# Optimization experiments

Measured on AMD Instinct MI355X. Metric: run time of the kernel, lower is better.

The kernel has to match this reference:

```python
import jax, jax.numpy as jnp
import numpy as np

B, CH_IN, CH_LAT, CLASSES, H, W = 4, 128, 128, 128, 1, 131072
BN_EPS = 1e-5
NEG_SLOPE = 0.01  # torch F.leaky_relu default


def setup_inputs() -> dict:
    key = jax.random.key(0)
    ks = jax.random.split(key, 12)
    x = jax.random.normal(ks[0], (B, CH_IN, H, W), jnp.float32)
    # 1x1 convs stored as [out_ch, in_ch]
    conv1_w = jax.random.normal(ks[1], (CH_LAT, CH_IN), jnp.float32) / np.sqrt(CH_IN).astype(np.float32)
    conv1_b = jax.random.normal(ks[2], (CH_LAT,), jnp.float32) * 0.1
    bn_gamma = jax.random.uniform(ks[3], (CH_LAT,), jnp.float32, 0.5, 1.5)
    bn_beta = jax.random.normal(ks[4], (CH_LAT,), jnp.float32) * 0.1
    bn_mean = jax.random.normal(ks[5], (CH_LAT,), jnp.float32) * 0.1
    bn_var = jax.random.uniform(ks[6], (CH_LAT,), jnp.float32, 0.5, 1.5)
    conv2_w = jax.random.normal(ks[7], (CLASSES + 1, CH_LAT), jnp.float32) / np.sqrt(CH_LAT).astype(np.float32)
    conv2_b = jax.random.normal(ks[8], (CLASSES + 1,), jnp.float32) * 0.1
    # CondMul: per-class weight [classes, in_feat] (output_features=1) + bias [classes]
    cm_w = jax.random.normal(ks[9], (CLASSES, CH_LAT), jnp.float32) / np.sqrt(CH_LAT).astype(np.float32)
    cm_b = jax.random.normal(ks[10], (CLASSES,), jnp.float32) * 0.1
    return {"x": x, "conv1_w": conv1_w, "conv1_b": conv1_b,
            "bn_gamma": bn_gamma, "bn_beta": bn_beta, "bn_mean": bn_mean, "bn_var": bn_var,
            "conv2_w": conv2_w, "conv2_b": conv2_b, "cm_w": cm_w, "cm_b": cm_b}


def reference(x, conv1_w, conv1_b, bn_gamma, bn_beta, bn_mean, bn_var,
              conv2_w, conv2_b, cm_w, cm_b):
    C = cm_w.shape[0]
    # conv_1 (1x1) + BatchNorm (eval, running stats) + LeakyReLU
    h = jnp.einsum('bchw,oc->bohw', x, conv1_w) + conv1_b[None, :, None, None]
    scale = bn_gamma * jax.lax.rsqrt(bn_var + BN_EPS)
    h = (h - bn_mean[None, :, None, None]) * scale[None, :, None, None] + bn_beta[None, :, None, None]
    x_latent = jnp.where(h >= 0, h, NEG_SLOPE * h)  # [B, CH_LAT, H, W]
    # conv_2 (1x1): classes logits + mask channel
    y = jnp.einsum('bchw,oc->bohw', x_latent, conv2_w) + conv2_b[None, :, None, None]
    cls_logits = y[:, :C]                              # [B, classes, H, W]
    m = y[:, -1:]
    mask = jnp.where(m >= 0, m, NEG_SLOPE * m)          # [B, 1, H, W]
    # tokens: transpose(1,3).reshape(-1, C) as in torch (valid since H==1)
    bsz, cl = x_latent.shape[0], x_latent.shape[1]
    x_l = jnp.transpose(x_latent, (0, 3, 2, 1)).reshape(-1, cl)  # [B*W*H, CH_LAT]
    inds = jnp.argmax(cls_logits, axis=1)               # [B, H, W] int
    idx = inds.reshape(-1)
    # CondMul: per-token class-indexed weight gather + dot product (irregular access)
    reg = jnp.sum(x_l * cm_w[idx], axis=1) + cm_b[idx]   # [B*H*W]
    reg = reg.reshape(bsz, 1, 1, -1)                     # [B, 1, 1, H*W]
    out = (inds[:, None].astype(jnp.float32) + reg) * (1.0 / float(C))
    return out, mask
```

## Files before the change

kernel.cpp:

```cpp
#include <hip/hip_runtime.h>
#include <math.h>

constexpr int CH   = 128;
constexpr int WW   = 131072;
constexpr int NB   = 4;
constexpr int NPIX = NB * WW;
constexpr int TPB  = 256;

constexpr int OFF_W1T = 0;
constexpr int OFF_BNA = 16384;
constexpr int OFF_BNC = 16512;
constexpr int OFF_W2G = 16640;
constexpr int OFF_WM  = 33024;

__global__ __launch_bounds__(256) void prep_kernel(
    const float* __restrict__ w1, const float* __restrict__ b1,
    const float* __restrict__ gamma, const float* __restrict__ beta,
    const float* __restrict__ mean, const float* __restrict__ var,
    const float* __restrict__ w2,
    float* __restrict__ ws)
{
    const int tid = threadIdx.x;
    for (int i = tid; i < CH * CH; i += 256) {
        const int c = i >> 7, o = i & 127;
        ws[OFF_W1T + c * CH + o] = w1[o * CH + c];
    }
    if (tid < CH) {
        const float s = gamma[tid] / sqrtf(var[tid] + 1e-5f);
        ws[OFF_BNA + tid] = s;
        ws[OFF_BNC + tid] = (b1[tid] - mean[tid]) * s + beta[tid];
        ws[OFF_WM  + tid] = w2[CH * CH + tid];
    }
    for (int i = tid; i < 16 * CH * 8; i += 256) {
        const int rg = i >> 10, r = i & 1023, c = r >> 3, j = r & 7;
        ws[OFF_W2G + i] = w2[(rg * 8 + j) * CH + c];
    }
}

__global__ __launch_bounds__(TPB, 2) void fused_kernel(
    const float* __restrict__ x,
    const float* __restrict__ b2,
    const float* __restrict__ cmw,
    const float* __restrict__ cmb,
    const float* __restrict__ ws,
    float* __restrict__ out)
{
    const int tid = threadIdx.x;
    const int p   = blockIdx.x * TPB + tid;
    const int b   = p >> 17;
    const int w   = p & (WW - 1);

    const float* __restrict__ w1t = ws + OFF_W1T;
    const float* __restrict__ bnA = ws + OFF_BNA;
    const float* __restrict__ bnC = ws + OFF_BNC;
    const float* __restrict__ w2g = ws + OFF_W2G;
    const float* __restrict__ wm  = ws + OFF_WM;

    float acc[CH];
    #pragma unroll
    for (int o = 0; o < CH; ++o) acc[o] = 0.f;

    const float* xc = x + ((size_t)b * CH) * WW + w;
    #pragma unroll 4
    for (int c = 0; c < CH; ++c) {
        const float xv = xc[(size_t)c * WW];
        const float* __restrict__ wr = w1t + c * CH;
        #pragma unroll
        for (int o = 0; o < CH; ++o)
            acc[o] = fmaf(xv, wr[o], acc[o]);
    }

    #pragma unroll
    for (int o = 0; o < CH; ++o) {
        const float v = fmaf(acc[o], bnA[o], bnC[o]);
        acc[o] = (v >= 0.f) ? v : 0.01f * v;
    }

    float best = -3.0e38f;
    int   bidx = 0;
    #pragma unroll 1
    for (int rg = 0; rg < 16; ++rg) {
        float y[8];
        #pragma unroll
        for (int j = 0; j < 8; ++j) y[j] = b2[rg * 8 + j];
        const float* __restrict__ wg = w2g + rg * (CH * 8);
        #pragma unroll
        for (int c = 0; c < CH; ++c) {
            #pragma unroll
            for (int j = 0; j < 8; ++j)
                y[j] = fmaf(acc[c], wg[c * 8 + j], y[j]);
        }
        #pragma unroll
        for (int j = 0; j < 8; ++j) {
            const bool g = y[j] > best;
            best = g ? y[j] : best;
            bidx = g ? rg * 8 + j : bidx;
        }
    }

    {
        float m = b2[CH];
        #pragma unroll
        for (int c = 0; c < CH; ++c)
            m = fmaf(acc[c], wm[c], m);
        out[NPIX + p] = (m >= 0.f) ? m : 0.01f * m;
    }

    {
        const float4* __restrict__ cr = (const float4*)(cmw + (size_t)bidx * CH);
        float r0 = 0.f, r1 = 0.f, r2 = 0.f, r3 = 0.f;
        #pragma unroll
        for (int c4 = 0; c4 < 32; ++c4) {
            const float4 v = cr[c4];
            r0 = fmaf(acc[c4*4+0], v.x, r0);
            r1 = fmaf(acc[c4*4+1], v.y, r1);
            r2 = fmaf(acc[c4*4+2], v.z, r2);
            r3 = fmaf(acc[c4*4+3], v.w, r3);
        }
        const float reg = ((r0 + r1) + (r2 + r3)) + cmb[bidx];
        out[p] = ((float)bidx + reg) * (1.0f / 128.0f);
    }
}

extern "C" void kernel_launch(void* const* d_in, const int* in_sizes, int n_in,
                              void* d_out, int out_size, void* d_ws, size_t ws_size,
                              hipStream_t stream) {
    const float* x     = (const float*)d_in[0];
    const float* w1    = (const float*)d_in[1];
    const float* b1    = (const float*)d_in[2];
    const float* gamma = (const float*)d_in[3];
    const float* beta  = (const float*)d_in[4];
    const float* mean  = (const float*)d_in[5];
    const float* var   = (const float*)d_in[6];
    const float* w2    = (const float*)d_in[7];
    const float* b2    = (const float*)d_in[8];
    const float* cmw   = (const float*)d_in[9];
    const float* cmb   = (const float*)d_in[10];
    float* ws  = (float*)d_ws;
    float* out = (float*)d_out;

    hipLaunchKernelGGL(prep_kernel, dim3(1), dim3(256), 0, stream,
                       w1, b1, gamma, beta, mean, var, w2, ws);
    hipLaunchKernelGGL(fused_kernel, dim3(NPIX / TPB), dim3(TPB), 0, stream,
                       x, b2, cmw, cmb, ws, out);
}
```

Before: 1.055 ms.

## Stage conv weights in LDS and prefetch input channels in groups of eight

Each block now copies both transposed 1x1-conv weight matrices (128 KB in total) into shared memory and reads them as float4 from LDS instead of through scalar global/constant loads. The input channel loop is restructured to software-prefetch the next eight channels while computing the current eight. Block size goes to 512 with occupancy 1, and the prep kernel is spread over 64 blocks. The 128 KB of LDS per block limits occupancy to one block per CU, and every block pays a fresh weight copy.

```diff
diff --git a/kernel.cpp b/kernel.cpp
--- a/kernel.cpp
+++ b/kernel.cpp
@@ -5,12 +5,12 @@
 constexpr int WW   = 131072;
 constexpr int NB   = 4;
 constexpr int NPIX = NB * WW;
-constexpr int TPB  = 256;
+constexpr int TPB  = 512;
 
 constexpr int OFF_W1T = 0;
-constexpr int OFF_BNA = 16384;
-constexpr int OFF_BNC = 16512;
-constexpr int OFF_W2G = 16640;
+constexpr int OFF_W2G = 16384;
+constexpr int OFF_BNA = 32768;
+constexpr int OFF_BNC = 32896;
 constexpr int OFF_WM  = 33024;
 
 __global__ __launch_bounds__(256) void prep_kernel(
@@ -20,24 +20,25 @@
     const float* __restrict__ w2,
     float* __restrict__ ws)
 {
-    const int tid = threadIdx.x;
-    for (int i = tid; i < CH * CH; i += 256) {
+    const int gid    = blockIdx.x * 256 + threadIdx.x;
+    const int stride = gridDim.x * 256;
+    for (int i = gid; i < CH * CH; i += stride) {
         const int c = i >> 7, o = i & 127;
         ws[OFF_W1T + c * CH + o] = w1[o * CH + c];
     }
-    if (tid < CH) {
-        const float s = gamma[tid] / sqrtf(var[tid] + 1e-5f);
-        ws[OFF_BNA + tid] = s;
-        ws[OFF_BNC + tid] = (b1[tid] - mean[tid]) * s + beta[tid];
-        ws[OFF_WM  + tid] = w2[CH * CH + tid];
-    }
-    for (int i = tid; i < 16 * CH * 8; i += 256) {
+    for (int i = gid; i < 16 * CH * 8; i += stride) {
         const int rg = i >> 10, r = i & 1023, c = r >> 3, j = r & 7;
         ws[OFF_W2G + i] = w2[(rg * 8 + j) * CH + c];
     }
+    if (gid < CH) {
+        const float s = gamma[gid] / sqrtf(var[gid] + 1e-5f);
+        ws[OFF_BNA + gid] = s;
+        ws[OFF_BNC + gid] = (b1[gid] - mean[gid]) * s + beta[gid];
+        ws[OFF_WM  + gid] = w2[CH * CH + gid];
+    }
 }
 
-__global__ __launch_bounds__(TPB, 2) void fused_kernel(
+__global__ __launch_bounds__(TPB, 1) void fused_kernel(
     const float* __restrict__ x,
     const float* __restrict__ b2,
     const float* __restrict__ cmw,
@@ -45,15 +46,29 @@
     const float* __restrict__ ws,
     float* __restrict__ out)
 {
+    __shared__ float lw1[CH * CH];
+    __shared__ float lw2[16 * CH * 8];
+
     const int tid = threadIdx.x;
-    const int p   = blockIdx.x * TPB + tid;
-    const int b   = p >> 17;
-    const int w   = p & (WW - 1);
 
-    const float* __restrict__ w1t = ws + OFF_W1T;
+    {
+        const float4* __restrict__ s1 = (const float4*)(ws + OFF_W1T);
+        float4* d1 = (float4*)lw1;
+        #pragma unroll
+        for (int k = 0; k < 8; ++k) d1[k * TPB + tid] = s1[k * TPB + tid];
+        const float4* __restrict__ s2 = (const float4*)(ws + OFF_W2G);
+        float4* d2 = (float4*)lw2;
+        #pragma unroll
+        for (int k = 0; k < 8; ++k) d2[k * TPB + tid] = s2[k * TPB + tid];
+    }
+    __syncthreads();
+
+    const int p = blockIdx.x * TPB + tid;
+    const int b = p >> 17;
+    const int w = p & (WW - 1);
+
     const float* __restrict__ bnA = ws + OFF_BNA;
     const float* __restrict__ bnC = ws + OFF_BNC;
-    const float* __restrict__ w2g = ws + OFF_W2G;
     const float* __restrict__ wm  = ws + OFF_WM;
 
     float acc[CH];
@@ -61,13 +76,42 @@
     for (int o = 0; o < CH; ++o) acc[o] = 0.f;
 
     const float* xc = x + ((size_t)b * CH) * WW + w;
-    #pragma unroll 4
-    for (int c = 0; c < CH; ++c) {
-        const float xv = xc[(size_t)c * WW];
-        const float* __restrict__ wr = w1t + c * CH;
+    float xa[8], xnx[8];
+    #pragma unroll
+    for (int k = 0; k < 8; ++k) xa[k] = xc[(size_t)k * WW];
+
+    #pragma unroll 1
+    for (int cg = 0; cg < CH - 8; cg += 8) {
         #pragma unroll
-        for (int o = 0; o < CH; ++o)
-            acc[o] = fmaf(xv, wr[o], acc[o]);
+        for (int k = 0; k < 8; ++k) xnx[k] = xc[(size_t)(cg + 8 + k) * WW];
+        #pragma unroll
+        for (int k = 0; k < 8; ++k) {
+            const float xv = xa[k];
+            const float4* __restrict__ wr = (const float4*)&lw1[(cg + k) * CH];
+            #pragma unroll
+            for (int o4 = 0; o4 < 32; ++o4) {
+                const float4 w4 = wr[o4];
+                acc[o4*4+0] = fmaf(xv, w4.x, acc[o4*4+0]);
+                acc[o4*4+1] = fmaf(xv, w4.y, acc[o4*4+1]);
+                acc[o4*4+2] = fmaf(xv, w4.z, acc[o4*4+2]);
+                acc[o4*4+3] = fmaf(xv, w4.w, acc[o4*4+3]);
+            }
+        }
+        #pragma unroll
+        for (int k = 0; k < 8; ++k) xa[k] = xnx[k];
+    }
+    #pragma unroll
+    for (int k = 0; k < 8; ++k) {
+        const float xv = xa[k];
+        const float4* __restrict__ wr = (const float4*)&lw1[(120 + k) * CH];
+        #pragma unroll
+        for (int o4 = 0; o4 < 32; ++o4) {
+            const float4 w4 = wr[o4];
+            acc[o4*4+0] = fmaf(xv, w4.x, acc[o4*4+0]);
+            acc[o4*4+1] = fmaf(xv, w4.y, acc[o4*4+1]);
+            acc[o4*4+2] = fmaf(xv, w4.z, acc[o4*4+2]);
+            acc[o4*4+3] = fmaf(xv, w4.w, acc[o4*4+3]);
+        }
     }
 
     #pragma unroll
@@ -83,12 +127,19 @@
         float y[8];
         #pragma unroll
         for (int j = 0; j < 8; ++j) y[j] = b2[rg * 8 + j];
-        const float* __restrict__ wg = w2g + rg * (CH * 8);
+        const float* __restrict__ wg = &lw2[rg * (CH * 8)];
         #pragma unroll
         for (int c = 0; c < CH; ++c) {
-            #pragma unroll
-            for (int j = 0; j < 8; ++j)
-                y[j] = fmaf(acc[c], wg[c * 8 + j], y[j]);
+            const float4 wa = *(const float4*)&wg[c * 8];
+            const float4 wb = *(const float4*)&wg[c * 8 + 4];
+            y[0] = fmaf(acc[c], wa.x, y[0]);
+            y[1] = fmaf(acc[c], wa.y, y[1]);
+            y[2] = fmaf(acc[c], wa.z, y[2]);
+            y[3] = fmaf(acc[c], wa.w, y[3]);
+            y[4] = fmaf(acc[c], wb.x, y[4]);
+            y[5] = fmaf(acc[c], wb.y, y[5]);
+            y[6] = fmaf(acc[c], wb.z, y[6]);
+            y[7] = fmaf(acc[c], wb.w, y[7]);
         }
         #pragma unroll
         for (int j = 0; j < 8; ++j) {
@@ -139,7 +190,7 @@
     float* ws  = (float*)d_ws;
     float* out = (float*)d_out;
 
-    hipLaunchKernelGGL(prep_kernel, dim3(1), dim3(256), 0, stream,
+    hipLaunchKernelGGL(prep_kernel, dim3(64), dim3(256), 0, stream,
                        w1, b1, gamma, beta, mean, var, w2, ws);
     hipLaunchKernelGGL(fused_kernel, dim3(NPIX / TPB), dim3(TPB), 0, stream,
                        x, b2, cmw, cmb, ws, out);
```

New measurement: 1.890 ms. +79.1%, slower.
